# Performance work log

Measured on AMD Instinct MI355X. Metric: run time of the kernel, lower is better.

The kernel has to match this reference:

```python
import jax, jax.numpy as jnp
import numpy as np

D_MODEL = 1024
HEADS = 16
Q_DIM = 1024
HEAD_DIM = Q_DIM // HEADS


def setup_inputs() -> dict:
    key = jax.random.key(0)
    ks = jax.random.split(key, 9)
    B, S = 2, 2048
    scale = 1.0 / np.sqrt(D_MODEL)
    inp = {
        "embeddings": jax.random.normal(ks[0], (B, S, D_MODEL), dtype=jnp.float32),
        "Wq": jax.random.normal(ks[1], (D_MODEL, Q_DIM), dtype=jnp.float32) * scale,
        "bq": jnp.zeros((Q_DIM,), dtype=jnp.float32),
        "Wk": jax.random.normal(ks[2], (D_MODEL, Q_DIM), dtype=jnp.float32) * scale,
        "bk": jnp.zeros((Q_DIM,), dtype=jnp.float32),
        "Wv": jax.random.normal(ks[3], (D_MODEL, Q_DIM), dtype=jnp.float32) * scale,
        "bv": jnp.zeros((Q_DIM,), dtype=jnp.float32),
        "Wo": jax.random.normal(ks[4], (Q_DIM, D_MODEL), dtype=jnp.float32) * scale,
        "bo": jnp.zeros((D_MODEL,), dtype=jnp.float32),
    }
    return inp


def reference(embeddings, Wq, bq, Wk, bk, Wv, bv, Wo, bo):
    B, S, _ = embeddings.shape
    # projections -> [B, H, S, Dh]
    def proj(W, b):
        x = embeddings @ W + b
        return x.reshape(B, S, HEADS, HEAD_DIM).transpose(0, 2, 1, 3)
    q = proj(Wq, bq)
    k = proj(Wk, bk)
    v = proj(Wv, bv)
    # scores scaled by sqrt(head_dim) as in source (no mask, dropout is no-op)
    scores = jnp.einsum("bhqd,bhkd->bhqk", q, k) / jnp.sqrt(
        jnp.asarray(HEAD_DIM, dtype=q.dtype)
    )
    p = jax.nn.softmax(scores, axis=-1)
    attn = jnp.einsum("bhqk,bhkd->bhqd", p, v)
    attn = attn.transpose(0, 2, 1, 3).reshape(B, S, Q_DIM)
    return attn @ Wo + bo
```

## Files before the change

### kernel.cpp

```cpp
#include <hip/hip_runtime.h>
#include <hip/hip_bf16.h>

#define BB 2
#define SS 2048
#define DMODEL 1024
#define NHEADS 16
#define DHEAD 64
#define MTOT (BB*SS)
#define NQKV 3072
#define QSCALE 0.18033688011112042f

typedef short bh8 __attribute__((ext_vector_type(8)));
typedef float fx4 __attribute__((ext_vector_type(4)));
typedef unsigned int ux2 __attribute__((ext_vector_type(2)));

__device__ __forceinline__ short f2bs(float f) {
    __hip_bfloat16 h = __float2bfloat16(f);
    return *reinterpret_cast<short*>(&h);
}

__device__ __forceinline__ unsigned pk_bf16(float a, float b) {
    __hip_bfloat162 h = __float22bfloat162_rn(make_float2(a, b));
    return *reinterpret_cast<unsigned*>(&h);
}

__device__ __forceinline__ void gload_lds16(const short* g, short* l) {
    __builtin_amdgcn_global_load_lds(
        (const __attribute__((address_space(1))) unsigned int*)g,
        (__attribute__((address_space(3))) unsigned int*)l, 16, 0, 0);
}

__global__ __launch_bounds__(256) void prep(
        const float* __restrict__ emb, short* __restrict__ Xbf,
        const float* __restrict__ Wq, const float* __restrict__ Wk,
        const float* __restrict__ Wv, const float* __restrict__ Wo,
        short* __restrict__ Wt_qkv, short* __restrict__ Wot) {
    __shared__ float tile[64][65];
    int bid = blockIdx.x, tid = threadIdx.x;
    if (bid < 4096) {
        int i = (bid * 256 + tid) * 4;
        float4 v = *(const float4*)(emb + i);
        short4 o;
        o.x = f2bs(v.x); o.y = f2bs(v.y); o.z = f2bs(v.z); o.w = f2bs(v.w);
        *(short4*)(Xbf + i) = o;
    } else {
        int b2 = bid - 4096;
        int bx = b2 & 15, by = (b2 >> 4) & 15, z = b2 >> 8;
        const float* src = (z == 0) ? Wq : (z == 1) ? Wk : (z == 2) ? Wv : Wo;
        short* dst = (z == 3) ? Wot : (Wt_qkv + (size_t)z * 1024 * 1024);
        int n0 = bx * 64, k0 = by * 64;
        int tx = tid & 63, ty = tid >> 6;
        for (int j = 0; j < 16; j++) {
            int r = ty + j * 4;
            tile[r][tx] = src[(size_t)(k0 + r) * 1024 + n0 + tx];
        }
        __syncthreads();
        for (int j = 0; j < 16; j++) {
            int r = ty + j * 4;
            dst[(size_t)(n0 + r) * 1024 + k0 + tx] = f2bs(tile[tx][r]);
        }
    }
}

template<int BM, int BN, int NN, int MODE>
__global__ __launch_bounds__(256) void gemm_bt_t(
        const short* __restrict__ A, const short* __restrict__ Bt,
        const float* __restrict__ bq, const float* __restrict__ bk,
        const float* __restrict__ bv, const float* __restrict__ bo,
        short* __restrict__ Qout, short* __restrict__ Kout,
        short* __restrict__ Vtout, float* __restrict__ Cout) {
    const int K = 1024;
    constexpr int ROWS = BM + BN;
    constexpr int CPW  = ROWS / 64;
    constexpr int MBK  = MTOT / BM;
    constexpr int STRIP = MBK / 8;
    constexpr int MT = BM / 32, NT = BN / 32;
    __shared__ __align__(16) short S[3][ROWS * 32];

    int tid = threadIdx.x;
    int w = tid >> 6, l = tid & 63, quad = l >> 4, ln = l & 15;
    int wm = w & 1, wn = w >> 1;

    int id = blockIdx.x;
    int xcd = id & 7, local = id >> 3;
    int mi = xcd * STRIP + (local % STRIP);
    int ni = local / STRIP;
    int m0 = mi * BM, n0 = ni * BN;

    const int which = (MODE == 0) ? (n0 >> 10) : 2;
    const bool swp = (MODE == 0) && (which != 2);

    const short* gsrc[CPW];
    int loff[CPW];
    #pragma unroll
    for (int j = 0; j < CPW; j++) {
        int r0 = (w * CPW + j) * 16;
        int row = r0 + (l >> 2);
        gsrc[j] = (r0 < BM ? A + (size_t)(m0 + row) * K
                           : Bt + (size_t)(n0 + row - BM) * K) + (l & 3) * 8;
        loff[j] = r0 * 32;
    }

    short *sC = &S[0][0], *sN = &S[1][0], *sN2 = &S[2][0];
    #pragma unroll
    for (int j = 0; j < CPW; j++) gload_lds16(gsrc[j], sC + loff[j]);
    #pragma unroll
    for (int j = 0; j < CPW; j++) gload_lds16(gsrc[j] + 32, sN + loff[j]);

    fx4 acc[MT][NT] = {};
    for (int it = 0; it < 32; ++it) {
        if (it < 31) {
            if constexpr (CPW == 4)
                asm volatile("s_waitcnt vmcnt(4)\n\ts_barrier" ::: "memory");
            else
                asm volatile("s_waitcnt vmcnt(3)\n\ts_barrier" ::: "memory");
        } else {
            asm volatile("s_waitcnt vmcnt(0)\n\ts_barrier" ::: "memory");
        }
        if (it < 30) {
            int k0 = (it + 2) * 32;
            #pragma unroll
            for (int j = 0; j < CPW; j++) gload_lds16(gsrc[j] + k0, sN2 + loff[j]);
        }
        bh8 af[MT], bf[NT];
        #pragma unroll
        for (int mt = 0; mt < MT; mt++)
            af[mt] = *(const bh8*)&sC[(wm * (BM / 2) + mt * 16 + ln) * 32 + quad * 8];
        #pragma unroll
        for (int nt = 0; nt < NT; nt++)
            bf[nt] = *(const bh8*)&sC[(BM + wn * (BN / 2) + nt * 16 + ln) * 32 + quad * 8];
        if (!swp) {
            #pragma unroll
            for (int mt = 0; mt < MT; mt++)
                #pragma unroll
                for (int nt = 0; nt < NT; nt++)
                    acc[mt][nt] = __builtin_amdgcn_mfma_f32_16x16x32_bf16(af[mt], bf[nt], acc[mt][nt], 0, 0, 0);
        } else {
            #pragma unroll
            for (int mt = 0; mt < MT; mt++)
                #pragma unroll
                for (int nt = 0; nt < NT; nt++)
                    acc[mt][nt] = __builtin_amdgcn_mfma_f32_16x16x32_bf16(bf[nt], af[mt], acc[mt][nt], 0, 0, 0);
        }
        short* t;
        t = sC; sC = sN; sN = sN2; sN2 = t;
    }

    if constexpr (MODE == 0) {
        int nbase = n0 + wn * 64;
        int nn0 = nbase & 1023;
        int h = nn0 >> 6;
        int mbase_w = m0 + wm * 64;
        int bb_ = mbase_w >> 11, s0 = mbase_w & 2047;

        if (which == 2) {
            #pragma unroll
            for (int nt = 0; nt < NT; nt++) {
                float bias = bv[nn0 + nt * 16 + ln];
                #pragma unroll
                for (int mt = 0; mt < MT; mt++)
                    #pragma unroll
                    for (int r = 0; r < 4; r++)
                        acc[mt][nt][r] += bias;
            }
            #pragma unroll
            for (int nt = 0; nt < NT; nt++) {
                int d = nt * 16 + ln;
                short* vrow = Vtout + ((size_t)(bb_ * 16 + h) * 64 + d) * 2048 + s0;
                #pragma unroll
                for (int mp = 0; mp < MT / 2; mp++) {
                    fx4 ea = acc[2 * mp][nt], eb = acc[2 * mp + 1][nt];
                    unsigned xa = pk_bf16(ea[0], ea[1]);
                    unsigned ya = pk_bf16(ea[2], ea[3]);
                    unsigned xb = pk_bf16(eb[0], eb[1]);
                    unsigned yb = pk_bf16(eb[2], eb[3]);
                    ux2 u   = __builtin_amdgcn_permlane32_swap(xa, xb, false, false);
                    ux2 d02 = __builtin_amdgcn_permlane16_swap(u.x, u.y, false, false);
                    ux2 u2  = __builtin_amdgcn_permlane32_swap(ya, yb, false, false);
                    ux2 d13 = __builtin_amdgcn_permlane16_swap(u2.x, u2.y, false, false);
                    union { unsigned u4[4]; uint4 v; } pk_;
                    pk_.u4[0] = d02.x; pk_.u4[1] = d13.x;
                    pk_.u4[2] = d02.y; pk_.u4[3] = d13.y;
                    *(uint4*)(vrow + (mp * 32 + quad * 8)) = pk_.v;
                }
            }
        } else {
            const float* bptr = (which == 0) ? bq : bk;
            float scl = (which == 0) ? QSCALE : 1.0f;
            short* out = (which == 0) ? Qout : Kout;
            asm volatile("s_waitcnt lgkmcnt(0)\n\ts_barrier" ::: "memory");
            float* PsF = (float*)&S[0][0] + w * 1088;
            int row = l >> 2, seg = l & 3;
            fx4 bjv[4];
            #pragma unroll
            for (int j = 0; j < 4; j++)
                bjv[j] = *(const fx4*)&bptr[nn0 + seg * 16 + j * 4];
            #pragma unroll
            for (int mt = 0; mt < MT; mt++) {
                #pragma unroll
                for (int nt = 0; nt < NT; nt++)
                    *(fx4*)&PsF[ln * 68 + nt * 16 + quad * 4] = acc[mt][nt];
                asm volatile("s_waitcnt lgkmcnt(0)" ::: "memory");
                int s_ = s0 + mt * 16 + row;
                short* crow = out + (((size_t)(bb_ * 16 + h) * 2048) + s_) * 64 + seg * 16;
                union { short sv[8]; uint4 u; } o0, o1;
                #pragma unroll
                for (int j = 0; j < 2; j++) {
                    fx4 v = *(const fx4*)&PsF[row * 68 + seg * 16 + j * 4];
                    o0.sv[j * 4 + 0] = f2bs((v[0] + bjv[j][0]) * scl);
                    o0.sv[j * 4 + 1] = f2bs((v[1] + bjv[j][1]) * scl);
                    o0.sv[j * 4 + 2] = f2bs((v[2] + bjv[j][2]) * scl);
                    o0.sv[j * 4 + 3] = f2bs((v[3] + bjv[j][3]) * scl);
                }
                #pragma unroll
                for (int j = 2; j < 4; j++) {
                    fx4 v = *(const fx4*)&PsF[row * 68 + seg * 16 + j * 4];
                    o1.sv[(j - 2) * 4 + 0] = f2bs((v[0] + bjv[j][0]) * scl);
                    o1.sv[(j - 2) * 4 + 1] = f2bs((v[1] + bjv[j][1]) * scl);
                    o1.sv[(j - 2) * 4 + 2] = f2bs((v[2] + bjv[j][2]) * scl);
                    o1.sv[(j - 2) * 4 + 3] = f2bs((v[3] + bjv[j][3]) * scl);
                }
                *(uint4*)&crow[0] = o0.u;
                *(uint4*)&crow[8] = o1.u;
                asm volatile("s_waitcnt lgkmcnt(0)" ::: "memory");
            }
        }
    } else {
        #pragma unroll
        for (int mt = 0; mt < MT; mt++) {
            #pragma unroll
            for (int nt = 0; nt < NT; nt++) {
                int n = n0 + wn * (BN / 2) + nt * 16 + ln;
                int mbase = m0 + wm * (BM / 2) + mt * 16 + quad * 4;
                #pragma unroll
                for (int r = 0; r < 4; r++) {
                    int m = mbase + r;
                    Cout[(size_t)m * 1024 + n] = acc[mt][nt][r] + bo[n];
                }
            }
        }
    }
}

__global__ __launch_bounds__(256, 4) void flash_attn(
        const short* __restrict__ Q, const short* __restrict__ Kg,
        const short* __restrict__ Vt, short* __restrict__ Ctx) {
    __shared__ __align__(16) short SH[16384];

    int tid = threadIdx.x;
    int w = tid >> 6, l = tid & 63, quad = l >> 4, ln = l & 15;
    int wq = w & 1, wk = w >> 1;
    int id = blockIdx.x;
    int xcd = id & 7, local = id >> 3;
    int bh = xcd * 4 + (local & 3);
    int qx = local >> 2;
    int qblk = qx * 64 + wq * 32;
    int b = bh >> 4, h = bh & 15;
    const short* Qb = Q  + (size_t)bh * 2048 * 64;
    const short* Kb = Kg + (size_t)bh * 2048 * 64;
    const short* Vb = Vt + (size_t)bh * 64 * 2048;
    int swz = ln & 7;

    bh8 qf[2][2];
    #pragma unroll
    for (int qt = 0; qt < 2; qt++)
        #pragma unroll
        for (int c = 0; c < 2; c++)
            qf[qt][c] = *(const bh8*)&Qb[(size_t)(qblk + qt * 16 + ln) * 64 + c * 32 + quad * 8];

    union { short s[8]; bh8 v; } one_;
    #pragma unroll
    for (int j = 0; j < 8; j++) one_.s[j] = 0x3F80;
    bh8 onesv = one_.v;

    const short* srcK[2]; const short* srcV[2]; int dstoff[2];
    #pragma unroll
    for (int j = 0; j < 2; j++) {
        int c = w * 2 + j;
        int row = c * 8 + (l >> 3);
        int pg = (l & 7) ^ (row & 7);
        srcK[j] = Kb + row * 64 + pg * 8;
        srcV[j] = Vb + (size_t)row * 2048 + pg * 8;
        dstoff[j] = c * 512;
    }

    #pragma unroll
    for (int j = 0; j < 2; j++) {
        gload_lds16(srcK[j], SH + dstoff[j]);
        gload_lds16(srcV[j], SH + 8192 + dstoff[j]);
    }

    fx4 o[2][4] = {};
    fx4 lacc[2] = {};

    for (int it = 0; it < 32; ++it) {
        int koff = (it & 1) ? 4096 : 0;
        asm volatile("s_waitcnt vmcnt(0) lgkmcnt(0)\n\ts_barrier" ::: "memory");
        if (it < 31) {
            int noff = koff ^ 4096;
            int kg = (it + 1) * 4096, vg = (it + 1) * 64;
            #pragma unroll
            for (int j = 0; j < 2; j++) {
                gload_lds16(srcK[j] + kg, SH + noff + dstoff[j]);
                gload_lds16(srcV[j] + vg, SH + 8192 + noff + dstoff[j]);
            }
        }
        const short* ksb = SH + koff;
        const short* vsb = SH + 8192 + koff;

        bh8 kf[2][2];
        #pragma unroll
        for (int mt = 0; mt < 2; mt++) {
            int krow = (wk * 32 + mt * 16 + ln) * 64;
            kf[mt][0] = *(const bh8*)&ksb[krow + ((quad ^ swz) * 8)];
            kf[mt][1] = *(const bh8*)&ksb[krow + (((quad + 4) ^ swz) * 8)];
        }
        fx4 s[2][2] = {};
        __builtin_amdgcn_s_setprio(1);
        #pragma unroll
        for (int mt = 0; mt < 2; mt++)
            #pragma unroll
            for (int qt = 0; qt < 2; qt++) {
                s[qt][mt] = __builtin_amdgcn_mfma_f32_16x16x32_bf16(kf[mt][0], qf[qt][0], s[qt][mt], 0, 0, 0);
                s[qt][mt] = __builtin_amdgcn_mfma_f32_16x16x32_bf16(kf[mt][1], qf[qt][1], s[qt][mt], 0, 0, 0);
            }
        __builtin_amdgcn_s_setprio(0);

        bh8 pf[2];
        #pragma unroll
        for (int qt = 0; qt < 2; qt++) {
            float e0[4], e1[4];
            #pragma unroll
            for (int r = 0; r < 4; r++) {
                e0[r] = __builtin_amdgcn_exp2f(s[qt][0][r]);
                e1[r] = __builtin_amdgcn_exp2f(s[qt][1][r]);
            }
            unsigned xa = pk_bf16(e0[0], e0[1]);
            unsigned ya = pk_bf16(e0[2], e0[3]);
            unsigned xb = pk_bf16(e1[0], e1[1]);
            unsigned yb = pk_bf16(e1[2], e1[3]);
            ux2 u   = __builtin_amdgcn_permlane32_swap(xa, xb, false, false);
            ux2 d02 = __builtin_amdgcn_permlane16_swap(u.x, u.y, false, false);
            ux2 u2  = __builtin_amdgcn_permlane32_swap(ya, yb, false, false);
            ux2 d13 = __builtin_amdgcn_permlane16_swap(u2.x, u2.y, false, false);
            union { unsigned u4[4]; bh8 v; } pk_;
            pk_.u4[0] = d02.x; pk_.u4[1] = d13.x;
            pk_.u4[2] = d02.y; pk_.u4[3] = d13.y;
            pf[qt] = pk_.v;
        }

        __builtin_amdgcn_s_setprio(1);
        #pragma unroll
        for (int dt = 0; dt < 4; dt++) {
            bh8 vf = *(const bh8*)&vsb[(dt * 16 + ln) * 64 + (((wk * 4 + quad) ^ swz) * 8)];
            o[0][dt] = __builtin_amdgcn_mfma_f32_16x16x32_bf16(vf, pf[0], o[0][dt], 0, 0, 0);
            o[1][dt] = __builtin_amdgcn_mfma_f32_16x16x32_bf16(vf, pf[1], o[1][dt], 0, 0, 0);
        }
        lacc[0] = __builtin_amdgcn_mfma_f32_16x16x32_bf16(onesv, pf[0], lacc[0], 0, 0, 0);
        lacc[1] = __builtin_amdgcn_mfma_f32_16x16x32_bf16(onesv, pf[1], lacc[1], 0, 0, 0);
        __builtin_amdgcn_s_setprio(0);
    }

    asm volatile("s_waitcnt vmcnt(0) lgkmcnt(0)\n\ts_barrier" ::: "memory");

    float* R  = (float*)SH + 2176;
    float* R2 = (float*)SH + 2176 + 4096;

    if (wk == 1) {
        float* Rw = R + wq * 2048;
        #pragma unroll
        for (int qt = 0; qt < 2; qt++)
            #pragma unroll
            for (int dt = 0; dt < 4; dt++)
                *(fx4*)&Rw[(((qt * 4 + dt) * 4 + quad) * 16 + ln) * 4] = o[qt][dt];
        if (quad == 0) {
            R2[wq * 32 + 0 * 16 + ln] = lacc[0][0];
            R2[wq * 32 + 1 * 16 + ln] = lacc[1][0];
        }
    }
    asm volatile("s_waitcnt lgkmcnt(0)\n\ts_barrier" ::: "memory");

    if (wk == 0) {
        float* Rw = R + wq * 2048;
        float linv[2];
        #pragma unroll
        for (int qt = 0; qt < 2; qt++) {
            #pragma unroll
            for (int dt = 0; dt < 4; dt++)
                o[qt][dt] += *(const fx4*)&Rw[(((qt * 4 + dt) * 4 + quad) * 16 + ln) * 4];
            float lf = lacc[qt][0] + R2[wq * 32 + qt * 16 + ln];
            linv[qt] = 1.0f / lf;
        }
        float* PsF = (float*)SH + wq * 1088;
        int row = l >> 2, seg = l & 3;
        #pragma unroll
        for (int qt = 0; qt < 2; qt++) {
            #pragma unroll
            for (int dt = 0; dt < 4; dt++)
                *(fx4*)&PsF[ln * 68 + dt * 16 + quad * 4] = o[qt][dt];
            asm volatile("s_waitcnt lgkmcnt(0)" ::: "memory");
            float invr = __shfl(linv[qt], row);
            int q = qblk + qt * 16 + row;
            short* crow = Ctx + ((size_t)(b * 2048 + q)) * 1024 + h * 64 + seg * 16;
            union { short s[8]; uint4 u; } o0, o1;
            #pragma unroll
            for (int j = 0; j < 2; j++) {
                fx4 v = *(const fx4*)&PsF[row * 68 + seg * 16 + j * 4];
                o0.s[j * 4 + 0] = f2bs(v[0] * invr);
                o0.s[j * 4 + 1] = f2bs(v[1] * invr);
                o0.s[j * 4 + 2] = f2bs(v[2] * invr);
                o0.s[j * 4 + 3] = f2bs(v[3] * invr);
            }
            #pragma unroll
            for (int j = 2; j < 4; j++) {
                fx4 v = *(const fx4*)&PsF[row * 68 + seg * 16 + j * 4];
                o1.s[(j - 2) * 4 + 0] = f2bs(v[0] * invr);
                o1.s[(j - 2) * 4 + 1] = f2bs(v[1] * invr);
                o1.s[(j - 2) * 4 + 2] = f2bs(v[2] * invr);
                o1.s[(j - 2) * 4 + 3] = f2bs(v[3] * invr);
            }
            *(uint4*)&crow[0] = o0.u;
            *(uint4*)&crow[8] = o1.u;
            asm volatile("s_waitcnt lgkmcnt(0)" ::: "memory");
        }
    }
}

extern "C" void kernel_launch(void* const* d_in, const int* in_sizes, int n_in,
                              void* d_out, int out_size, void* d_ws, size_t ws_size,
                              hipStream_t stream) {
    const float* emb = (const float*)d_in[0];
    const float* Wq  = (const float*)d_in[1];
    const float* bq  = (const float*)d_in[2];
    const float* Wk  = (const float*)d_in[3];
    const float* bk  = (const float*)d_in[4];
    const float* Wv  = (const float*)d_in[5];
    const float* bv  = (const float*)d_in[6];
    const float* Wo  = (const float*)d_in[7];
    const float* bo  = (const float*)d_in[8];

    char* ws = (char*)d_ws;
    const size_t MB = 1024 * 1024;
    short* Xbf  = (short*)(ws + 0);
    short* Ctx  = (short*)(ws + 0);
    short* Wt   = (short*)(ws + 8 * MB);
    short* Wot  = (short*)(ws + 17 * MB);
    short* Qb   = (short*)(ws + 19 * MB);
    short* Kb   = (short*)(ws + 27 * MB);
    short* Vtb  = (short*)(ws + 35 * MB);

    prep<<<5120, 256, 0, stream>>>(emb, Xbf, Wq, Wk, Wv, Wo, Wt, Wot);
    gemm_bt_t<128, 128, NQKV, 0><<<768, 256, 0, stream>>>(
        Xbf, Wt, bq, bk, bv, nullptr, Qb, Kb, Vtb, nullptr);
    flash_attn<<<1024, 256, 0, stream>>>(Qb, Kb, Vtb, Ctx);
    gemm_bt_t<64, 128, DMODEL, 1><<<512, 256, 0, stream>>>(
        Ctx, Wot, nullptr, nullptr, nullptr, bo, nullptr, nullptr, nullptr, (float*)d_out);
}
```

Before: 198.3 us.

## Use swapped MFMA layout for Q/K/out-proj epilogues with vectorized stores

Enables the swapped operand order for the output projection GEMM and uses it for the Q/K epilogue. This removes the LDS staging round-trip and its barrier in the Q/K store path, replacing it with register-level permlane packing into 16-byte stores. The output projection now writes float4 rows with vector-loaded bias instead of scalar strided stores. The prep kernel's weight transpose also writes short4 instead of single shorts. Correctness depends on the swapped accumulator layout matching the new indexing.

```diff
diff --git a/kernel.cpp b/kernel.cpp
--- a/kernel.cpp
+++ b/kernel.cpp
@@ -22,6 +22,20 @@
 __device__ __forceinline__ unsigned pk_bf16(float a, float b) {
     __hip_bfloat162 h = __float22bfloat162_rn(make_float2(a, b));
     return *reinterpret_cast<unsigned*>(&h);
+}
+
+__device__ __forceinline__ uint4 pack32(fx4 ea, fx4 eb) {
+    unsigned xa = pk_bf16(ea[0], ea[1]);
+    unsigned ya = pk_bf16(ea[2], ea[3]);
+    unsigned xb = pk_bf16(eb[0], eb[1]);
+    unsigned yb = pk_bf16(eb[2], eb[3]);
+    ux2 u   = __builtin_amdgcn_permlane32_swap(xa, xb, false, false);
+    ux2 d02 = __builtin_amdgcn_permlane16_swap(u.x, u.y, false, false);
+    ux2 u2  = __builtin_amdgcn_permlane32_swap(ya, yb, false, false);
+    ux2 d13 = __builtin_amdgcn_permlane16_swap(u2.x, u2.y, false, false);
+    uint4 r;
+    r.x = d02.x; r.y = d13.x; r.z = d02.y; r.w = d13.y;
+    return r;
 }
 
 __device__ __forceinline__ void gload_lds16(const short* g, short* l) {
@@ -55,9 +69,16 @@
             tile[r][tx] = src[(size_t)(k0 + r) * 1024 + n0 + tx];
         }
         __syncthreads();
-        for (int j = 0; j < 16; j++) {
-            int r = ty + j * 4;
-            dst[(size_t)(n0 + r) * 1024 + k0 + tx] = f2bs(tile[tx][r]);
+        int c4 = tid & 15, rr = tid >> 4;
+        #pragma unroll
+        for (int pass = 0; pass < 4; pass++) {
+            int r = rr + pass * 16;
+            short4 o;
+            o.x = f2bs(tile[c4 * 4 + 0][r]);
+            o.y = f2bs(tile[c4 * 4 + 1][r]);
+            o.z = f2bs(tile[c4 * 4 + 2][r]);
+            o.w = f2bs(tile[c4 * 4 + 3][r]);
+            *(short4*)&dst[(size_t)(n0 + r) * 1024 + k0 + c4 * 4] = o;
         }
     }
 }
@@ -88,7 +109,7 @@
     int m0 = mi * BM, n0 = ni * BN;
 
     const int which = (MODE == 0) ? (n0 >> 10) : 2;
-    const bool swp = (MODE == 0) && (which != 2);
+    const bool swp = (MODE == 1) || (which != 2);
 
     const short* gsrc[CPW];
     int loff[CPW];
@@ -169,74 +190,49 @@
                 short* vrow = Vtout + ((size_t)(bb_ * 16 + h) * 64 + d) * 2048 + s0;
                 #pragma unroll
                 for (int mp = 0; mp < MT / 2; mp++) {
-                    fx4 ea = acc[2 * mp][nt], eb = acc[2 * mp + 1][nt];
-                    unsigned xa = pk_bf16(ea[0], ea[1]);
-                    unsigned ya = pk_bf16(ea[2], ea[3]);
-                    unsigned xb = pk_bf16(eb[0], eb[1]);
-                    unsigned yb = pk_bf16(eb[2], eb[3]);
-                    ux2 u   = __builtin_amdgcn_permlane32_swap(xa, xb, false, false);
-                    ux2 d02 = __builtin_amdgcn_permlane16_swap(u.x, u.y, false, false);
-                    ux2 u2  = __builtin_amdgcn_permlane32_swap(ya, yb, false, false);
-                    ux2 d13 = __builtin_amdgcn_permlane16_swap(u2.x, u2.y, false, false);
-                    union { unsigned u4[4]; uint4 v; } pk_;
-                    pk_.u4[0] = d02.x; pk_.u4[1] = d13.x;
-                    pk_.u4[2] = d02.y; pk_.u4[3] = d13.y;
-                    *(uint4*)(vrow + (mp * 32 + quad * 8)) = pk_.v;
+                    uint4 pk = pack32(acc[2 * mp][nt], acc[2 * mp + 1][nt]);
+                    *(uint4*)(vrow + (mp * 32 + quad * 8)) = pk;
                 }
             }
         } else {
             const float* bptr = (which == 0) ? bq : bk;
             float scl = (which == 0) ? QSCALE : 1.0f;
             short* out = (which == 0) ? Qout : Kout;
-            asm volatile("s_waitcnt lgkmcnt(0)\n\ts_barrier" ::: "memory");
-            float* PsF = (float*)&S[0][0] + w * 1088;
-            int row = l >> 2, seg = l & 3;
-            fx4 bjv[4];
-            #pragma unroll
-            for (int j = 0; j < 4; j++)
-                bjv[j] = *(const fx4*)&bptr[nn0 + seg * 16 + j * 4];
+            fx4 bv4[NT];
+            #pragma unroll
+            for (int nt = 0; nt < NT; nt++)
+                bv4[nt] = *(const fx4*)&bptr[nn0 + nt * 16 + quad * 4];
+            #pragma unroll
+            for (int mt = 0; mt < MT; mt++)
+                #pragma unroll
+                for (int nt = 0; nt < NT; nt++)
+                    #pragma unroll
+                    for (int r = 0; r < 4; r++)
+                        acc[mt][nt][r] = (acc[mt][nt][r] + bv4[nt][r]) * scl;
             #pragma unroll
             for (int mt = 0; mt < MT; mt++) {
-                #pragma unroll
-                for (int nt = 0; nt < NT; nt++)
-                    *(fx4*)&PsF[ln * 68 + nt * 16 + quad * 4] = acc[mt][nt];
-                asm volatile("s_waitcnt lgkmcnt(0)" ::: "memory");
-                int s_ = s0 + mt * 16 + row;
-                short* crow = out + (((size_t)(bb_ * 16 + h) * 2048) + s_) * 64 + seg * 16;
-                union { short sv[8]; uint4 u; } o0, o1;
-                #pragma unroll
-                for (int j = 0; j < 2; j++) {
-                    fx4 v = *(const fx4*)&PsF[row * 68 + seg * 16 + j * 4];
-                    o0.sv[j * 4 + 0] = f2bs((v[0] + bjv[j][0]) * scl);
-                    o0.sv[j * 4 + 1] = f2bs((v[1] + bjv[j][1]) * scl);
-                    o0.sv[j * 4 + 2] = f2bs((v[2] + bjv[j][2]) * scl);
-                    o0.sv[j * 4 + 3] = f2bs((v[3] + bjv[j][3]) * scl);
+                int s_ = s0 + mt * 16 + ln;
+                short* crow = out + (((size_t)(bb_ * 16 + h) * 2048) + s_) * 64;
+                #pragma unroll
+                for (int np = 0; np < NT / 2; np++) {
+                    uint4 pk = pack32(acc[mt][2 * np], acc[mt][2 * np + 1]);
+                    *(uint4*)(crow + (np * 32 + quad * 8)) = pk;
                 }
-                #pragma unroll
-                for (int j = 2; j < 4; j++) {
-                    fx4 v = *(const fx4*)&PsF[row * 68 + seg * 16 + j * 4];
-                    o1.sv[(j - 2) * 4 + 0] = f2bs((v[0] + bjv[j][0]) * scl);
-                    o1.sv[(j - 2) * 4 + 1] = f2bs((v[1] + bjv[j][1]) * scl);
-                    o1.sv[(j - 2) * 4 + 2] = f2bs((v[2] + bjv[j][2]) * scl);
-                    o1.sv[(j - 2) * 4 + 3] = f2bs((v[3] + bjv[j][3]) * scl);
-                }
-                *(uint4*)&crow[0] = o0.u;
-                *(uint4*)&crow[8] = o1.u;
-                asm volatile("s_waitcnt lgkmcnt(0)" ::: "memory");
             }
         }
     } else {
+        int nbase = n0 + wn * (BN / 2);
+        fx4 bv4[NT];
+        #pragma unroll
+        for (int nt = 0; nt < NT; nt++)
+            bv4[nt] = *(const fx4*)&bo[nbase + nt * 16 + quad * 4];
         #pragma unroll
         for (int mt = 0; mt < MT; mt++) {
+            int m = m0 + wm * (BM / 2) + mt * 16 + ln;
             #pragma unroll
             for (int nt = 0; nt < NT; nt++) {
-                int n = n0 + wn * (BN / 2) + nt * 16 + ln;
-                int mbase = m0 + wm * (BM / 2) + mt * 16 + quad * 4;
-                #pragma unroll
-                for (int r = 0; r < 4; r++) {
-                    int m = mbase + r;
-                    Cout[(size_t)m * 1024 + n] = acc[mt][nt][r] + bo[n];
-                }
+                fx4 v = acc[mt][nt] + bv4[nt];
+                *(fx4*)&Cout[(size_t)m * 1024 + nbase + nt * 16 + quad * 4] = v;
             }
         }
     }
@@ -329,24 +325,16 @@
         bh8 pf[2];
         #pragma unroll
         for (int qt = 0; qt < 2; qt++) {
-            float e0[4], e1[4];
+            fx4 e0, e1;
             #pragma unroll
             for (int r = 0; r < 4; r++) {
                 e0[r] = __builtin_amdgcn_exp2f(s[qt][0][r]);
                 e1[r] = __builtin_amdgcn_exp2f(s[qt][1][r]);
             }
-            unsigned xa = pk_bf16(e0[0], e0[1]);
-            unsigned ya = pk_bf16(e0[2], e0[3]);
-            unsigned xb = pk_bf16(e1[0], e1[1]);
-            unsigned yb = pk_bf16(e1[2], e1[3]);
-            ux2 u   = __builtin_amdgcn_permlane32_swap(xa, xb, false, false);
-            ux2 d02 = __builtin_amdgcn_permlane16_swap(u.x, u.y, false, false);
-            ux2 u2  = __builtin_amdgcn_permlane32_swap(ya, yb, false, false);
-            ux2 d13 = __builtin_amdgcn_permlane16_swap(u2.x, u2.y, false, false);
-            union { unsigned u4[4]; bh8 v; } pk_;
-            pk_.u4[0] = d02.x; pk_.u4[1] = d13.x;
-            pk_.u4[2] = d02.y; pk_.u4[3] = d13.y;
-            pf[qt] = pk_.v;
+            uint4 pk = pack32(e0, e1);
+            union { uint4 u; bh8 v; } pc;
+            pc.u = pk;
+            pf[qt] = pc.v;
         }
 
         __builtin_amdgcn_s_setprio(1);
```

New measurement: 205.7 us. 3.8% more time.
